# Optimization experiments

Hardware: AMD Instinct MI355X
Metric: run time of the kernel (lower is better)

Reference implementation:

```python
import jax, jax.numpy as jnp
import numpy as np

# Mex config (matches init_kwargs)
B, C, H, W = 64, 64, 64, 64
BLK = (64, 3, 3)        # block over (C, H, W); spans all channels -> out_c = 1
STR = (64, 2, 2)
PAD = (0, 1, 1)
NI = 256                # num_instances
EPS = 1.0
SOFTMAX_MODE = False    # False -> mean (logsumexp - log k), True -> plain logsumexp


def setup_inputs() -> dict:
    key = jax.random.key(0)
    k1, k2 = jax.random.split(key)
    x = jax.random.normal(k1, (B, C, H, W), dtype=jnp.float32)
    kblk = BLK[0] * BLK[1] * BLK[2]
    # Dirichlet([1]*k) init == normalized exponentials; nregions = 1 (shared offsets)
    e = jax.random.exponential(k2, (1, NI, kblk), dtype=jnp.float32)
    offsets = (e / jnp.sum(e, axis=-1, keepdims=True)).reshape(1, NI, *BLK)
    return {"x": x, "offsets": offsets}


def _mex_forward(x, offsets):
    eps = jnp.float32(EPS)
    bc, bh, bw = BLK
    # im2col patch extraction: (B, C*bh*bw, OH, OW); feature dim ordered (c, fh, fw)
    patches = jax.lax.conv_general_dilated_patches(
        x, (bh, bw), (STR[1], STR[2]),
        [(PAD[1], PAD[1]), (PAD[2], PAD[2])],  # zero padding == blocks_out_of_bounds_value
        dimension_numbers=("NCHW", "OIHW", "NCHW"),
    )
    Bn, K, OH, OW = patches.shape  # K = bc*bh*bw = 576
    P = patches.transpose(0, 2, 3, 1).reshape(-1, K)  # (N, k), N = B*OH*OW
    O = offsets.reshape(NI, K)                         # single shared region

    # y_ni = (1/eps) * logsumexp_k( eps*(P_nk + O_ik) ) - log(k)/eps (mean mode)
    # exp-domain GEMM with max-shift for stability:
    Pe = eps * P
    Oe = eps * O
    mp = jnp.max(Pe, axis=1, keepdims=True)   # (N, 1)
    mo = jnp.max(Oe, axis=1, keepdims=True)   # (I, 1)
    S = jnp.exp(Pe - mp) @ jnp.exp(Oe - mo).T  # (N, I)
    y = (jnp.log(S) + mp + mo.T) / eps
    if not SOFTMAX_MODE:
        y = y - jnp.log(jnp.float32(K)) / eps
    # output: (B, num_instances * out_c, OH, OW) with out_c = 1
    return y.reshape(Bn, OH, OW, NI).transpose(0, 3, 1, 2)


def reference(x, offsets):
    return _mex_forward(x, offsets)
```

## Files before the change

kernel.cpp:

```cpp
#include <hip/hip_runtime.h>
#include <hip/hip_bf16.h>


typedef __bf16 bf16x8 __attribute__((ext_vector_type(8)));
typedef float  f32x4  __attribute__((ext_vector_type(4)));

__global__ void mex_prep_b(const float* __restrict__ off, __bf16* __restrict__ Bt) {
    const int i = blockIdx.x * 4 + (threadIdx.x >> 6);
    const int c = threadIdx.x & 63;
    const int c8 = c >> 3, j = c & 7;
    const int wv = i >> 6, nt = (i >> 4) & 3, t16 = i & 15;
    const int q  = c8 & 3;
    const float* oi = off + i * 576;
    #pragma unroll
    for (int p = 0; p < 9; ++p) {
        float v = oi[c * 9 + p];
        const int ks    = p * 2 + (c8 >> 2);
        const int chunk = (ks * 16 + wv * 4 + nt) * 64 + q * 16 + t16;
        Bt[chunk * 8 + j] = (__bf16)__expf(v);
    }
}

__global__ __launch_bounds__(256, 2) void mex_main(
        const float* __restrict__ x,
        const __bf16* __restrict__ Bt,
        float* __restrict__ out) {
    __shared__ bf16x8 lds8[2 * 2560];

    const int bid = blockIdx.x;
    const int wid  = ((bid & 7) << 6) | (bid >> 3);
    const int b    = wid >> 3;
    const int j2   = wid & 7;
    const int oh0a = j2 << 2;
    const int oh0b = oh0a + 2;
    const int tid  = threadIdx.x;
    const int wv   = tid >> 6;
    const int lane = tid & 63;

    bf16x8 one8;
    #pragma unroll
    for (int j = 0; j < 8; ++j) one8[j] = (__bf16)1.0f;

    if (oh0a == 0) {
        #pragma unroll
        for (int i = 0; i < 2; ++i) lds8[tid + i * 256] = one8;
    }

    const int wp  = tid & 31;
    const int w0  = wp << 1;
    const int c8  = tid >> 5;
    const int c8p = c8 ^ (wp & 7);
    const float* xb = x + ((size_t)b << 18) + w0;

    #pragma unroll
    for (int hl = 0; hl < 5; ++hl) {
        const int hg = 2 * oh0a - 1 + hl;
        if (hg >= 0) {
            const float* xp = xb + (hg << 6);
            float2 v[8];
            #pragma unroll
            for (int k = 0; k < 8; ++k)
                v[k] = *(const float2*)(xp + (((c8 << 3) + k) << 12));
            bf16x8 ca, cb;
            #pragma unroll
            for (int k = 0; k < 8; ++k) {
                ca[k] = (__bf16)__expf(v[k].x);
                cb[k] = (__bf16)__expf(v[k].y);
            }
            bf16x8* dst = lds8 + hl * 512 + w0 * 8 + c8p;
            dst[0] = ca;
            dst[8] = cb;
        }
    }

    float2 v1[40];
    #pragma unroll
    for (int hl = 0; hl < 5; ++hl) {
        const int hg = 2 * oh0b - 1 + hl;
        const float* xp = xb + (hg << 6);
        #pragma unroll
        for (int k = 0; k < 8; ++k)
            v1[hl * 8 + k] = *(const float2*)(xp + (((c8 << 3) + k) << 12));
    }

    const bf16x8* __restrict__ Btv = (const bf16x8*)Bt;
    const int wv4 = wv << 2;
    bf16x8 bcur[4];
    #pragma unroll
    for (int nt = 0; nt < 4; ++nt)
        bcur[nt] = Btv[(wv4 + nt) * 64 + lane];

    const int t16 = tid & 15;
    const int q   = (tid >> 4) & 3;
    int hb[4], wo2[4];
    #pragma unroll
    for (int mt = 0; mt < 4; ++mt) {
        const int m = mt * 16 + t16;
        wo2[mt] = (m & 31) << 1;
        hb[mt]  = (m >> 5) << 7;
    }
    const float lK = 6.356107660695891f;

    auto kloop = [&](const bf16x8* __restrict__ L, f32x4 (&acc)[4][4],
                     bf16x8 (&bc)[4]) {
        #pragma unroll
        for (int ks = 0; ks < 18; ++ks) {
            const int p  = ks >> 1;
            const int fh = (p * 11) >> 5;
            const int fw = p - fh * 3;
            const int ccq = ((ks & 1) << 2) + q;
            bf16x8 a[4];
            #pragma unroll
            for (int mt = 0; mt < 4; ++mt) {
                const int wc  = wo2[mt] + fw - 1;
                const int pad = wc < 0;
                const int wcl = pad ? 0 : wc;
                const int row = hb[mt] + fh * 64 + wcl;
                bf16x8 vv = L[row * 8 + (ccq ^ ((wcl >> 1) & 7))];
                a[mt] = pad ? one8 : vv;
            }
            bf16x8 bnext[4];
            if (ks < 17) {
                #pragma unroll
                for (int nt = 0; nt < 4; ++nt)
                    bnext[nt] = Btv[((ks + 1) * 16 + wv4 + nt) * 64 + lane];
            }
            #pragma unroll
            for (int mt = 0; mt < 4; ++mt)
                #pragma unroll
                for (int nt = 0; nt < 4; ++nt)
                    acc[mt][nt] = __builtin_amdgcn_mfma_f32_16x16x32_bf16(
                        a[mt], bc[nt], acc[mt][nt], 0, 0, 0);
            #pragma unroll
            for (int nt = 0; nt < 4; ++nt) bc[nt] = bnext[nt];
        }
    };

    auto epilogue = [&](f32x4 (&acc)[4][4], int oh0) {
        #pragma unroll
        for (int mt = 0; mt < 4; ++mt) {
            const int m   = mt * 16 + (q << 2);
            const int ohl = m >> 5;
            const int owi = m & 31;
            const int orow = (oh0 + ohl) * 32 + owi;
            #pragma unroll
            for (int nt = 0; nt < 4; ++nt) {
                const int inst = wv * 64 + nt * 16 + t16;
                f32x4 r;
                #pragma unroll
                for (int j = 0; j < 4; ++j)
                    r[j] = __logf(acc[mt][nt][j]) - lK;
                *(f32x4*)(out + (((size_t)b * 256 + inst) * 1024 + orow)) = r;
            }
        }
    };

    __syncthreads();

    f32x4 acc0[4][4];
    #pragma unroll
    for (int mt = 0; mt < 4; ++mt)
        #pragma unroll
        for (int nt = 0; nt < 4; ++nt) acc0[mt][nt] = (f32x4)(0.0f);
    kloop(lds8, acc0, bcur);

    #pragma unroll
    for (int hl = 0; hl < 5; ++hl) {
        bf16x8 ca, cb;
        #pragma unroll
        for (int k = 0; k < 8; ++k) {
            ca[k] = (__bf16)__expf(v1[hl * 8 + k].x);
            cb[k] = (__bf16)__expf(v1[hl * 8 + k].y);
        }
        bf16x8* dst = lds8 + 2560 + hl * 512 + w0 * 8 + c8p;
        dst[0] = ca;
        dst[8] = cb;
    }
    #pragma unroll
    for (int nt = 0; nt < 4; ++nt)
        bcur[nt] = Btv[(wv4 + nt) * 64 + lane];

    __syncthreads();

    epilogue(acc0, oh0a);

    f32x4 acc1[4][4];
    #pragma unroll
    for (int mt = 0; mt < 4; ++mt)
        #pragma unroll
        for (int nt = 0; nt < 4; ++nt) acc1[mt][nt] = (f32x4)(0.0f);
    kloop(lds8 + 2560, acc1, bcur);

    epilogue(acc1, oh0b);
}

extern "C" void kernel_launch(void* const* d_in, const int* in_sizes, int n_in,
                              void* d_out, int out_size, void* d_ws, size_t ws_size,
                              hipStream_t stream) {
    const float* x   = (const float*)d_in[0];
    const float* off = (const float*)d_in[1];
    float* out = (float*)d_out;
    __bf16* Bt = (__bf16*)d_ws;

    mex_prep_b<<<64, 256, 0, stream>>>(off, Bt);
    mex_main<<<512, 256, 0, stream>>>(x, Bt, out);
}
```

Measured before the change: 143.8 us.

## Halve per-block output tile to one row per phase, doubling grid size

Each block now computes two single output rows (32 pixels each) instead of two 2-row tiles, with the M dimension cut from 64 to 32 per phase and LDS staging shrunk from 5 to 3 input rows. The grid doubles to 1024 blocks and launch bounds allow 3 blocks per CU, aiming for more occupancy and better load balance across CUs. In exchange, overlapping input halo rows are loaded and exponentiated more often relative to the output produced, and each B-fragment load from global memory feeds half as many MFMAs.

```diff
diff --git a/kernel.cpp b/kernel.cpp
--- a/kernel.cpp
+++ b/kernel.cpp
@@ -21,18 +21,17 @@
     }
 }
 
-__global__ __launch_bounds__(256, 2) void mex_main(
+__global__ __launch_bounds__(256, 3) void mex_main(
         const float* __restrict__ x,
         const __bf16* __restrict__ Bt,
         float* __restrict__ out) {
-    __shared__ bf16x8 lds8[2 * 2560];
+    __shared__ bf16x8 lds8[2 * 1536];
 
     const int bid = blockIdx.x;
-    const int wid  = ((bid & 7) << 6) | (bid >> 3);
-    const int b    = wid >> 3;
-    const int j2   = wid & 7;
-    const int oh0a = j2 << 2;
-    const int oh0b = oh0a + 2;
+    const int wid  = ((bid & 7) << 7) | (bid >> 3);
+    const int b    = wid >> 4;
+    const int oh_a = (wid & 15) << 1;
+    const int oh_b = oh_a + 1;
     const int tid  = threadIdx.x;
     const int wv   = tid >> 6;
     const int lane = tid & 63;
@@ -41,7 +40,7 @@
     #pragma unroll
     for (int j = 0; j < 8; ++j) one8[j] = (__bf16)1.0f;
 
-    if (oh0a == 0) {
+    if (oh_a == 0) {
         #pragma unroll
         for (int i = 0; i < 2; ++i) lds8[tid + i * 256] = one8;
     }
@@ -53,8 +52,8 @@
     const float* xb = x + ((size_t)b << 18) + w0;
 
     #pragma unroll
-    for (int hl = 0; hl < 5; ++hl) {
-        const int hg = 2 * oh0a - 1 + hl;
+    for (int hl = 0; hl < 3; ++hl) {
+        const int hg = 2 * oh_a - 1 + hl;
         if (hg >= 0) {
             const float* xp = xb + (hg << 6);
             float2 v[8];
@@ -73,11 +72,10 @@
         }
     }
 
-    float2 v1[40];
-    #pragma unroll
-    for (int hl = 0; hl < 5; ++hl) {
-        const int hg = 2 * oh0b - 1 + hl;
-        const float* xp = xb + (hg << 6);
+    float2 v1[24];
+    #pragma unroll
+    for (int hl = 0; hl < 3; ++hl) {
+        const float* xp = xb + ((2 * oh_a + 1 + hl) << 6);
         #pragma unroll
         for (int k = 0; k < 8; ++k)
             v1[hl * 8 + k] = *(const float2*)(xp + (((c8 << 3) + k) << 12));
@@ -92,16 +90,13 @@
 
     const int t16 = tid & 15;
     const int q   = (tid >> 4) & 3;
-    int hb[4], wo2[4];
-    #pragma unroll
-    for (int mt = 0; mt < 4; ++mt) {
-        const int m = mt * 16 + t16;
-        wo2[mt] = (m & 31) << 1;
-        hb[mt]  = (m >> 5) << 7;
-    }
+    int wo2[2];
+    #pragma unroll
+    for (int mt = 0; mt < 2; ++mt)
+        wo2[mt] = (mt * 16 + t16) << 1;
     const float lK = 6.356107660695891f;
 
-    auto kloop = [&](const bf16x8* __restrict__ L, f32x4 (&acc)[4][4],
+    auto kloop = [&](const bf16x8* __restrict__ L, f32x4 (&acc)[2][4],
                      bf16x8 (&bc)[4]) {
         #pragma unroll
         for (int ks = 0; ks < 18; ++ks) {
@@ -109,13 +104,13 @@
             const int fh = (p * 11) >> 5;
             const int fw = p - fh * 3;
             const int ccq = ((ks & 1) << 2) + q;
-            bf16x8 a[4];
-            #pragma unroll
-            for (int mt = 0; mt < 4; ++mt) {
+            bf16x8 a[2];
+            #pragma unroll
+            for (int mt = 0; mt < 2; ++mt) {
                 const int wc  = wo2[mt] + fw - 1;
                 const int pad = wc < 0;
                 const int wcl = pad ? 0 : wc;
-                const int row = hb[mt] + fh * 64 + wcl;
+                const int row = fh * 64 + wcl;
                 bf16x8 vv = L[row * 8 + (ccq ^ ((wcl >> 1) & 7))];
                 a[mt] = pad ? one8 : vv;
             }
@@ -126,7 +121,7 @@
                     bnext[nt] = Btv[((ks + 1) * 16 + wv4 + nt) * 64 + lane];
             }
             #pragma unroll
-            for (int mt = 0; mt < 4; ++mt)
+            for (int mt = 0; mt < 2; ++mt)
                 #pragma unroll
                 for (int nt = 0; nt < 4; ++nt)
                     acc[mt][nt] = __builtin_amdgcn_mfma_f32_16x16x32_bf16(
@@ -136,13 +131,11 @@
         }
     };
 
-    auto epilogue = [&](f32x4 (&acc)[4][4], int oh0) {
-        #pragma unroll
-        for (int mt = 0; mt < 4; ++mt) {
-            const int m   = mt * 16 + (q << 2);
-            const int ohl = m >> 5;
-            const int owi = m & 31;
-            const int orow = (oh0 + ohl) * 32 + owi;
+    auto epilogue = [&](f32x4 (&acc)[2][4], int oh) {
+        #pragma unroll
+        for (int mt = 0; mt < 2; ++mt) {
+            const int owi  = mt * 16 + (q << 2);
+            const int orow = (oh << 5) + owi;
             #pragma unroll
             for (int nt = 0; nt < 4; ++nt) {
                 const int inst = wv * 64 + nt * 16 + t16;
@@ -157,22 +150,22 @@
 
     __syncthreads();
 
-    f32x4 acc0[4][4];
-    #pragma unroll
-    for (int mt = 0; mt < 4; ++mt)
+    f32x4 acc0[2][4];
+    #pragma unroll
+    for (int mt = 0; mt < 2; ++mt)
         #pragma unroll
         for (int nt = 0; nt < 4; ++nt) acc0[mt][nt] = (f32x4)(0.0f);
     kloop(lds8, acc0, bcur);
 
     #pragma unroll
-    for (int hl = 0; hl < 5; ++hl) {
+    for (int hl = 0; hl < 3; ++hl) {
         bf16x8 ca, cb;
         #pragma unroll
         for (int k = 0; k < 8; ++k) {
             ca[k] = (__bf16)__expf(v1[hl * 8 + k].x);
             cb[k] = (__bf16)__expf(v1[hl * 8 + k].y);
         }
-        bf16x8* dst = lds8 + 2560 + hl * 512 + w0 * 8 + c8p;
+        bf16x8* dst = lds8 + 1536 + hl * 512 + w0 * 8 + c8p;
         dst[0] = ca;
         dst[8] = cb;
     }
@@ -182,16 +175,16 @@
 
     __syncthreads();
 
-    epilogue(acc0, oh0a);
-
-    f32x4 acc1[4][4];
-    #pragma unroll
-    for (int mt = 0; mt < 4; ++mt)
+    epilogue(acc0, oh_a);
+
+    f32x4 acc1[2][4];
+    #pragma unroll
+    for (int mt = 0; mt < 2; ++mt)
         #pragma unroll
         for (int nt = 0; nt < 4; ++nt) acc1[mt][nt] = (f32x4)(0.0f);
-    kloop(lds8 + 2560, acc1, bcur);
-
-    epilogue(acc1, oh0b);
+    kloop(lds8 + 1536, acc1, bcur);
+
+    epilogue(acc1, oh_b);
 }
 
 extern "C" void kernel_launch(void* const* d_in, const int* in_sizes, int n_in,
@@ -203,5 +196,5 @@
     __bf16* Bt = (__bf16*)d_ws;
 
     mex_prep_b<<<64, 256, 0, stream>>>(off, Bt);
-    mex_main<<<512, 256, 0, stream>>>(x, Bt, out);
+    mex_main<<<1024, 256, 0, stream>>>(x, Bt, out);
 }
```

Result: slower. 188.9 us (+31.3%).
